# Optimization experiments

Hardware: AMD Instinct MI355X
Metric: run time of the kernel (lower is better)

## Reference

```python
import jax, jax.numpy as jnp
import numpy as np

# Standard JPEG luminance quantization table (quality 50)
_QTABLE = np.array([
    [16, 11, 10, 16, 24, 40, 51, 61],
    [12, 12, 14, 19, 26, 58, 60, 55],
    [14, 13, 16, 24, 40, 57, 69, 56],
    [14, 17, 22, 29, 51, 87, 80, 62],
    [18, 22, 37, 56, 68, 109, 103, 77],
    [24, 35, 55, 64, 81, 104, 113, 92],
    [49, 64, 78, 87, 103, 121, 120, 101],
    [72, 92, 95, 98, 112, 100, 103, 99]], dtype=np.float32)

def _dct_mtx(n=8):
    # Orthonormal DCT-II basis matrix: mtx @ block @ mtx.T is the 2-D DCT,
    # so mtx.T @ coeffs @ mtx is the inverse DCT used by this module.
    k = np.arange(n)[:, None]
    j = np.arange(n)[None, :]
    m = np.cos(np.pi * (2 * j + 1) * k / (2 * n)) * np.sqrt(2.0 / n)
    m[0, :] /= np.sqrt(2.0)
    return m.astype(np.float32)

def setup_inputs() -> dict:
    key = jax.random.key(0)
    B, C, H, W = 32, 1, 1024, 1024  # square image required by the reshape chain
    x = jax.random.normal(key, (B, C, H, W), dtype=jnp.float32) * 10.0
    return {
        "x": x,
        "qtable": jnp.asarray(_QTABLE),
        "mtx": jnp.asarray(_dct_mtx(8)),
    }

def reference(x, qtable, mtx):
    B, D1, D2, D3 = x.shape
    # view -> permute -> reshape chain extracting 8x8 blocks (faithful to torch code)
    y = x.reshape(B, D1 * D2 // 8, 8, D3)
    y = jnp.transpose(y, (0, 1, 3, 2))                       # (B, D1*D2/8, D3, 8)
    y = y.reshape(B, D1 * D2 * D3 // 64, 8, 8)
    y = jnp.transpose(y, (0, 1, 3, 2))                       # (B, Nblk, 8, 8)
    y = y * qtable                                           # dequantize
    # mtx.T @ y @ mtx  (batched tiny 8x8 IDCT)
    y = jnp.einsum('ji,bnjk,kl->bnil', mtx, y, mtx)
    # inverse reshape/permute chain back to image layout
    y = jnp.transpose(y, (0, 1, 3, 2))
    y = y.reshape(B, D1 * D2 // 8, D2, 8)
    y = jnp.transpose(y, (0, 1, 3, 2))
    return y.reshape(x.shape) + 128.0
```

## Files before the change

### kernel.cpp

```cpp
#include <hip/hip_runtime.h>


typedef float f32x4 __attribute__((ext_vector_type(4)));

__global__ __launch_bounds__(256, 8) void bidct_kernel(
    const float* __restrict__ x, const float* __restrict__ qt,
    const float* __restrict__ mtx, float* __restrict__ out)
{
    __shared__ float4 tile4[4][136];

    const int wv = threadIdx.x >> 6;
    const int l  = threadIdx.x & 63;
    float4* __restrict__ tw = tile4[wv];

    const int wid  = blockIdx.x * 4 + wv;
    const int img  = wid >> 11;
    const int rest = wid & 2047;
    const int rg   = rest >> 4;
    const int cg   = rest & 15;
    const size_t base = ((size_t)img << 20) + ((size_t)rg << 13) + ((size_t)cg << 6);

#pragma unroll
    for (int r = 0; r < 2; ++r) {
        const int f  = r * 64 + l;
        const int j  = f >> 4;
        const int c4 = f & 15;
        const float4 v = *reinterpret_cast<const float4*>(x + base + j * 1024 + c4 * 4);
        tw[j * 17 + c4] = v;
    }

    const int bl = l >> 3;
    const int i  = l & 7;

    float mcol[8];
#pragma unroll
    for (int j = 0; j < 8; ++j) mcol[j] = mtx[j * 8 + i];

    float T[8] = {0.f, 0.f, 0.f, 0.f, 0.f, 0.f, 0.f, 0.f};
#pragma unroll
    for (int j = 0; j < 8; ++j) {
        const float4 xa = tw[j * 17 + bl * 2];
        const float4 xb = tw[j * 17 + bl * 2 + 1];
        const float mj = mcol[j];
        T[0] = fmaf(mj, xa.x * qt[j * 8 + 0], T[0]);
        T[1] = fmaf(mj, xa.y * qt[j * 8 + 1], T[1]);
        T[2] = fmaf(mj, xa.z * qt[j * 8 + 2], T[2]);
        T[3] = fmaf(mj, xa.w * qt[j * 8 + 3], T[3]);
        T[4] = fmaf(mj, xb.x * qt[j * 8 + 4], T[4]);
        T[5] = fmaf(mj, xb.y * qt[j * 8 + 5], T[5]);
        T[6] = fmaf(mj, xb.z * qt[j * 8 + 6], T[6]);
        T[7] = fmaf(mj, xb.w * qt[j * 8 + 7], T[7]);
    }

    float o[8] = {128.f, 128.f, 128.f, 128.f, 128.f, 128.f, 128.f, 128.f};
#pragma unroll
    for (int k = 0; k < 8; ++k) {
        const float tk = T[k];
#pragma unroll
        for (int lcol = 0; lcol < 8; ++lcol)
            o[lcol] = fmaf(tk, mtx[k * 8 + lcol], o[lcol]);
    }

    tw[i * 17 + bl * 2]     = make_float4(o[0], o[1], o[2], o[3]);
    tw[i * 17 + bl * 2 + 1] = make_float4(o[4], o[5], o[6], o[7]);

#pragma unroll
    for (int r = 0; r < 2; ++r) {
        const int f  = r * 64 + l;
        const int j  = f >> 4;
        const int c4 = f & 15;
        const float4 v = tw[j * 17 + c4];
        f32x4 nv; nv.x = v.x; nv.y = v.y; nv.z = v.z; nv.w = v.w;
        __builtin_nontemporal_store(nv,
            reinterpret_cast<f32x4*>(out + base + j * 1024 + c4 * 4));
    }
}

extern "C" void kernel_launch(void* const* d_in, const int* in_sizes, int n_in,
                              void* d_out, int out_size, void* d_ws, size_t ws_size,
                              hipStream_t stream) {
    const float* x   = (const float*)d_in[0];
    const float* qt  = (const float*)d_in[1];
    const float* mtx = (const float*)d_in[2];
    float*       out = (float*)d_out;

    const int grid = out_size / 2048;
    bidct_kernel<<<grid, 256, 0, stream>>>(x, qt, mtx, out);
}
```

Baseline: 230.1 us.

## Process full 8-row image bands per block with a persistent two-band loop

Each block now loads a whole 8x1024 row band (128 blocks of 8x8) into a padded shared tile, with each thread issuing 8 float4 loads at a 4KB stride. Each wave then runs the IDCT on 32 blocks, and the block does two bands in sequence. The aim is more memory-level parallelism per thread and longer contiguous rows per access, in exchange for about 32KB of shared memory and fewer resident blocks. Correctness relies on each wave touching only its own columns of the tile, which is why no barriers are needed.

```diff
diff --git a/kernel.cpp b/kernel.cpp
--- a/kernel.cpp
+++ b/kernel.cpp
@@ -3,76 +3,77 @@
 
 typedef float f32x4 __attribute__((ext_vector_type(4)));
 
-__global__ __launch_bounds__(256, 8) void bidct_kernel(
+__global__ __launch_bounds__(256, 4) void bidct_kernel(
     const float* __restrict__ x, const float* __restrict__ qt,
     const float* __restrict__ mtx, float* __restrict__ out)
 {
-    __shared__ float4 tile4[4][136];
+    __shared__ float tile[8 * 1028];
 
-    const int wv = threadIdx.x >> 6;
-    const int l  = threadIdx.x & 63;
-    float4* __restrict__ tw = tile4[wv];
-
-    const int wid  = blockIdx.x * 4 + wv;
-    const int img  = wid >> 11;
-    const int rest = wid & 2047;
-    const int rg   = rest >> 4;
-    const int cg   = rest & 15;
-    const size_t base = ((size_t)img << 20) + ((size_t)rg << 13) + ((size_t)cg << 6);
-
-#pragma unroll
-    for (int r = 0; r < 2; ++r) {
-        const int f  = r * 64 + l;
-        const int j  = f >> 4;
-        const int c4 = f & 15;
-        const float4 v = *reinterpret_cast<const float4*>(x + base + j * 1024 + c4 * 4);
-        tw[j * 17 + c4] = v;
-    }
-
-    const int bl = l >> 3;
+    const int t  = threadIdx.x;
+    const int wv = t >> 6;
+    const int l  = t & 63;
+    const int b3 = l >> 3;
     const int i  = l & 7;
+    const int c4 = wv * 64 + l;
 
     float mcol[8];
 #pragma unroll
     for (int j = 0; j < 8; ++j) mcol[j] = mtx[j * 8 + i];
 
-    float T[8] = {0.f, 0.f, 0.f, 0.f, 0.f, 0.f, 0.f, 0.f};
+    for (int s = 0; s < 2; ++s) {
+        const int band = blockIdx.x * 2 + s;
+        const size_t base = (size_t)band * 8192;
+
+        float4 v[8];
 #pragma unroll
-    for (int j = 0; j < 8; ++j) {
-        const float4 xa = tw[j * 17 + bl * 2];
-        const float4 xb = tw[j * 17 + bl * 2 + 1];
-        const float mj = mcol[j];
-        T[0] = fmaf(mj, xa.x * qt[j * 8 + 0], T[0]);
-        T[1] = fmaf(mj, xa.y * qt[j * 8 + 1], T[1]);
-        T[2] = fmaf(mj, xa.z * qt[j * 8 + 2], T[2]);
-        T[3] = fmaf(mj, xa.w * qt[j * 8 + 3], T[3]);
-        T[4] = fmaf(mj, xb.x * qt[j * 8 + 4], T[4]);
-        T[5] = fmaf(mj, xb.y * qt[j * 8 + 5], T[5]);
-        T[6] = fmaf(mj, xb.z * qt[j * 8 + 6], T[6]);
-        T[7] = fmaf(mj, xb.w * qt[j * 8 + 7], T[7]);
-    }
-
-    float o[8] = {128.f, 128.f, 128.f, 128.f, 128.f, 128.f, 128.f, 128.f};
+        for (int k = 0; k < 8; ++k)
+            v[k] = *reinterpret_cast<const float4*>(x + base + k * 1024 + c4 * 4);
 #pragma unroll
-    for (int k = 0; k < 8; ++k) {
-        const float tk = T[k];
-#pragma unroll
-        for (int lcol = 0; lcol < 8; ++lcol)
-            o[lcol] = fmaf(tk, mtx[k * 8 + lcol], o[lcol]);
-    }
-
-    tw[i * 17 + bl * 2]     = make_float4(o[0], o[1], o[2], o[3]);
-    tw[i * 17 + bl * 2 + 1] = make_float4(o[4], o[5], o[6], o[7]);
+        for (int k = 0; k < 8; ++k)
+            *reinterpret_cast<float4*>(&tile[k * 1028 + c4 * 4]) = v[k];
 
 #pragma unroll
-    for (int r = 0; r < 2; ++r) {
-        const int f  = r * 64 + l;
-        const int j  = f >> 4;
-        const int c4 = f & 15;
-        const float4 v = tw[j * 17 + c4];
-        f32x4 nv; nv.x = v.x; nv.y = v.y; nv.z = v.z; nv.w = v.w;
-        __builtin_nontemporal_store(nv,
-            reinterpret_cast<f32x4*>(out + base + j * 1024 + c4 * 4));
+        for (int p = 0; p < 4; ++p) {
+            const int B = wv * 32 + p * 8 + b3;
+
+            float T[8] = {0.f, 0.f, 0.f, 0.f, 0.f, 0.f, 0.f, 0.f};
+#pragma unroll
+            for (int j = 0; j < 8; ++j) {
+                const float4 xa = *reinterpret_cast<const float4*>(&tile[j * 1028 + B * 8]);
+                const float4 xb = *reinterpret_cast<const float4*>(&tile[j * 1028 + B * 8 + 4]);
+                const float mj = mcol[j];
+                T[0] = fmaf(mj, xa.x * qt[j * 8 + 0], T[0]);
+                T[1] = fmaf(mj, xa.y * qt[j * 8 + 1], T[1]);
+                T[2] = fmaf(mj, xa.z * qt[j * 8 + 2], T[2]);
+                T[3] = fmaf(mj, xa.w * qt[j * 8 + 3], T[3]);
+                T[4] = fmaf(mj, xb.x * qt[j * 8 + 4], T[4]);
+                T[5] = fmaf(mj, xb.y * qt[j * 8 + 5], T[5]);
+                T[6] = fmaf(mj, xb.z * qt[j * 8 + 6], T[6]);
+                T[7] = fmaf(mj, xb.w * qt[j * 8 + 7], T[7]);
+            }
+
+            float o[8] = {128.f, 128.f, 128.f, 128.f, 128.f, 128.f, 128.f, 128.f};
+#pragma unroll
+            for (int k = 0; k < 8; ++k) {
+                const float tk = T[k];
+#pragma unroll
+                for (int lc = 0; lc < 8; ++lc)
+                    o[lc] = fmaf(tk, mtx[k * 8 + lc], o[lc]);
+            }
+
+            *reinterpret_cast<float4*>(&tile[i * 1028 + B * 8])     =
+                make_float4(o[0], o[1], o[2], o[3]);
+            *reinterpret_cast<float4*>(&tile[i * 1028 + B * 8 + 4]) =
+                make_float4(o[4], o[5], o[6], o[7]);
+        }
+
+#pragma unroll
+        for (int k = 0; k < 8; ++k) {
+            const float4 w4 = *reinterpret_cast<const float4*>(&tile[k * 1028 + c4 * 4]);
+            f32x4 nv; nv.x = w4.x; nv.y = w4.y; nv.z = w4.z; nv.w = w4.w;
+            __builtin_nontemporal_store(nv,
+                reinterpret_cast<f32x4*>(out + base + k * 1024 + c4 * 4));
+        }
     }
 }
 
@@ -84,6 +85,7 @@
     const float* mtx = (const float*)d_in[2];
     float*       out = (float*)d_out;
 
-    const int grid = out_size / 2048;
+    const int bands = out_size / 8192;
+    const int grid  = bands / 2;
     bidct_kernel<<<grid, 256, 0, stream>>>(x, qt, mtx, out);
 }
```

Result: slower. 241.1 us (+4.8%).
